# Performance work log

Measured on AMD Instinct MI355X. Metric: run time of the kernel, lower is better.

Reference implementation:

```python
import jax, jax.numpy as jnp
import numpy as np

FA, FB_CAT, FM, HID = 133, 147, 8, 100  # atom feat, bond feat (concat), mol feat, hidden
N_ATOMS, N_BONDS, N_MOLS, MAX_NB = 250000, 500000, 10000, 6
DEPTH = 3


def setup_inputs() -> dict:
    key = jax.random.key(0)
    ks = jax.random.split(key, 10)
    f_atoms = jax.random.normal(ks[0], (N_ATOMS, FA), jnp.float32)
    f_bonds = jax.random.normal(ks[1], (N_BONDS, FB_CAT), jnp.float32)
    f_mol = jax.random.normal(ks[2], (N_MOLS, FM), jnp.float32)
    a2b = jax.random.randint(ks[3], (N_ATOMS, MAX_NB), 0, N_BONDS, jnp.int32)
    b2a = jax.random.randint(ks[4], (N_BONDS,), 0, N_ATOMS, jnp.int32)
    b2revb = jax.random.randint(ks[5], (N_BONDS,), 0, N_BONDS, jnp.int32)
    # contiguous molecules of 25 atoms each -> equivalent of ascope segments
    mol_id = (jnp.arange(N_ATOMS, dtype=jnp.int32) // (N_ATOMS // N_MOLS))
    # parameters (Linear with bias=False): stored as (in, out)
    W_i = jax.random.normal(ks[6], (FB_CAT, HID), jnp.float32) * 0.05
    W_h = jax.random.normal(ks[7], (HID, HID), jnp.float32) * 0.05
    W_o = jax.random.normal(ks[8], (HID + FA, HID), jnp.float32) * 0.05
    return {"f_atoms": f_atoms, "f_bonds": f_bonds, "f_mol": f_mol,
            "W_i": W_i, "W_h": W_h, "W_o": W_o,
            "a2b": a2b, "b2a": b2a, "b2revb": b2revb,
            "mol_id": mol_id, "n_mols": N_MOLS}


def reference(f_atoms, f_bonds, f_mol, W_i, W_h, W_o, a2b, b2a, b2revb, mol_id, n_mols):
    act = jax.nn.relu
    inp = act(f_bonds @ W_i)              # (B, H)
    message = inp
    for _ in range(DEPTH - 1):
        nei = message[a2b]                # (A, MAX_NB, H) gather
        a_message = nei.sum(axis=1)       # (A, H)
        message = a_message[b2a] - message[b2revb]  # (B, H)
        message = act(inp + message @ W_h)
        # dropout p=0 (eval) -> identity
    # readout to atoms
    a_message = message[a2b].sum(axis=1)  # (A, H)
    a_input = jnp.concatenate([f_atoms, a_message], axis=1)  # (A, FA+H)
    atom_hiddens = act(a_input @ W_o)     # (A, H)
    # per-molecule mean over ragged segments (ascope equivalent)
    mol_sum = jax.ops.segment_sum(atom_hiddens, mol_id, num_segments=n_mols)
    counts = jax.ops.segment_sum(jnp.ones((atom_hiddens.shape[0],), atom_hiddens.dtype),
                                 mol_id, num_segments=n_mols)
    mol_vecs = mol_sum / jnp.maximum(counts, 1.0)[:, None]  # zero-vec for empty mols
    mol_vecs = jnp.concatenate([mol_vecs, f_mol], axis=1)   # (M, H+FM)
    return mol_vecs, atom_hiddens
```

## Files before the change

### kernel.cpp

```cpp
#include <hip/hip_runtime.h>

#define THREADS 256
#define MS 128

typedef __bf16 bf16x8 __attribute__((ext_vector_type(8)));
typedef float f32x4 __attribute__((ext_vector_type(4)));
typedef float f32x4u __attribute__((ext_vector_type(4), aligned(4)));

__device__ __forceinline__ unsigned short f2b(float x) {
    unsigned int u = __float_as_uint(x);
    u = (u + 0x7FFFu + ((u >> 16) & 1u)) >> 16;
    return (unsigned short)u;
}
__device__ __forceinline__ float b2f(unsigned short h) {
    return __uint_as_float(((unsigned int)h) << 16);
}
__device__ __forceinline__ bf16x8 as_bf(uint4 q) {
    union { uint4 q; bf16x8 v; } u; u.q = q; return u.v;
}

__global__ __launch_bounds__(64) void pack_w(const float* __restrict__ W,
                                             unsigned short* __restrict__ out, int K)
{
    int bid = blockIdx.x;
    int kc = bid / 7, nt = bid - kc * 7;
    int l = threadIdx.x;
    int k0 = kc * 32 + (l >> 4) * 8;
    int n = nt * 16 + (l & 15);
    unsigned short v[8];
    #pragma unroll
    for (int j = 0; j < 8; ++j) {
        int k = k0 + j;
        float x = (k < K && n < 100) ? W[(size_t)k * 100 + n] : 0.f;
        v[j] = f2b(x);
    }
    *(uint4*)&out[((size_t)bid * 64 + l) * 8] = *(uint4*)v;
}

__global__ __launch_bounds__(64) void pack_wo(const float* __restrict__ W,
                                              unsigned short* __restrict__ out)
{
    int bid = blockIdx.x;
    int kc = bid / 7, nt = bid - kc * 7;
    int l = threadIdx.x;
    int k0 = kc * 32 + (l >> 4) * 8;
    int n = nt * 16 + (l & 15);
    unsigned short v[8];
    #pragma unroll
    for (int j = 0; j < 8; ++j) {
        int k = k0 + j;
        float x = 0.f;
        if (n < 100) {
            if (k < 100)                 x = W[(size_t)(133 + k) * 100 + n];
            else if (k >= 112 && k < 245) x = W[(size_t)(k - 112) * 100 + n];
        }
        v[j] = f2b(x);
    }
    *(uint4*)&out[((size_t)bid * 64 + l) * 8] = *(uint4*)v;
}

__global__ __launch_bounds__(THREADS) void gather_sum_bf16(
    const unsigned short* __restrict__ msg, const int* __restrict__ a2b,
    unsigned short* __restrict__ amsg, int A)
{
    int t = blockIdx.x * THREADS + threadIdx.x;
    if (t >= A * 16) return;
    int a = t >> 4;
    int c = t & 15;
    if (c >= 14) {
        *(uint4*)&amsg[(size_t)a * MS + c * 8] = make_uint4(0u, 0u, 0u, 0u);
        return;
    }
    const int* nb = a2b + (size_t)a * 6;
    float s[8];
    #pragma unroll
    for (int e = 0; e < 8; ++e) s[e] = 0.f;
    #pragma unroll
    for (int j = 0; j < 6; ++j) {
        uint4 v = *(const uint4*)&msg[(size_t)nb[j] * MS + c * 8];
        const unsigned short* pv = (const unsigned short*)&v;
        #pragma unroll
        for (int e = 0; e < 8; ++e) s[e] += b2f(pv[e]);
    }
    unsigned short r[8];
    #pragma unroll
    for (int e = 0; e < 8; ++e) r[e] = f2b(s[e]);
    *(uint4*)&amsg[(size_t)a * MS + c * 8] = *(uint4*)r;
}

__global__ __launch_bounds__(THREADS) void gemm_in(
    const float* __restrict__ fb, const unsigned short* __restrict__ wf,
    unsigned short* __restrict__ Y, int M)
{
    __shared__ unsigned short Os[64 * 136];
    const int tid = threadIdx.x;
    const int l = tid & 63, w = tid >> 6;
    const int quad = l >> 4, c15 = l & 15;
    const int row0 = blockIdx.x * 64;
    const int rc = min(row0 + w * 16 + c15, M - 1);
    const float* rowp = fb + (size_t)rc * 147;

    uint4 af[5];
    #pragma unroll
    for (int kc = 0; kc < 4; ++kc) {
        f32x4u x0 = *(const f32x4u*)(rowp + kc * 32 + quad * 8);
        f32x4u x1 = *(const f32x4u*)(rowp + kc * 32 + quad * 8 + 4);
        unsigned short t[8];
        #pragma unroll
        for (int e = 0; e < 4; ++e) { t[e] = f2b(x0[e]); t[4 + e] = f2b(x1[e]); }
        af[kc] = *(uint4*)t;
    }
    {
        unsigned short t[8];
        #pragma unroll
        for (int j = 0; j < 8; ++j) {
            int k = 128 + quad * 8 + j;
            t[j] = (k < 147) ? f2b(rowp[k]) : (unsigned short)0;
        }
        af[4] = *(uint4*)t;
    }

    f32x4 acc[7];
    #pragma unroll
    for (int nt = 0; nt < 7; ++nt) acc[nt] = (f32x4){0.f, 0.f, 0.f, 0.f};
    #pragma unroll
    for (int kc = 0; kc < 5; ++kc) {
        #pragma unroll
        for (int nt = 0; nt < 7; ++nt) {
            uint4 bq = *(const uint4*)&wf[((size_t)(kc * 7 + nt) * 64 + l) * 8];
            acc[nt] = __builtin_amdgcn_mfma_f32_16x16x32_bf16(as_bf(af[kc]), as_bf(bq), acc[nt], 0, 0, 0);
        }
    }

    #pragma unroll
    for (int nt = 0; nt < 7; ++nt)
        #pragma unroll
        for (int reg = 0; reg < 4; ++reg)
            Os[(w * 16 + quad * 4 + reg) * 136 + nt * 16 + c15] = f2b(fmaxf(acc[nt][reg], 0.f));
    __syncthreads();

    for (int t = tid; t < 64 * 16; t += THREADS) {
        int rl = t >> 4, c = t & 15;
        int rr = row0 + rl;
        if (rr < M) {
            uint4 o = (c < 14) ? *(const uint4*)&Os[rl * 136 + c * 8]
                               : make_uint4(0u, 0u, 0u, 0u);
            *(uint4*)&Y[(size_t)rr * MS + c * 8] = o;
        }
    }
}

__global__ __launch_bounds__(THREADS) void gemm_msg(
    const unsigned short* __restrict__ amsg, const unsigned short* __restrict__ msg,
    const int* __restrict__ b2a, const int* __restrict__ b2revb,
    const unsigned short* __restrict__ wf, const unsigned short* __restrict__ bias,
    unsigned short* __restrict__ Y, int M)
{
    __shared__ unsigned short Os[64 * 136];
    const int tid = threadIdx.x;
    const int l = tid & 63, w = tid >> 6;
    const int quad = l >> 4, c15 = l & 15;
    const int row0 = blockIdx.x * 64;
    const int rc = min(row0 + w * 16 + c15, M - 1);
    const int iA = b2a[rc], iB = b2revb[rc];
    const unsigned short* pa = amsg + (size_t)iA * MS + quad * 8;
    const unsigned short* pb = msg  + (size_t)iB * MS + quad * 8;

    uint4 a1[4], a2[4];
    #pragma unroll
    for (int kc = 0; kc < 4; ++kc) {
        a1[kc] = *(const uint4*)(pa + kc * 32);
        a2[kc] = *(const uint4*)(pb + kc * 32);
    }

    f32x4 acc1[7], acc2[7];
    #pragma unroll
    for (int nt = 0; nt < 7; ++nt) {
        acc1[nt] = (f32x4){0.f, 0.f, 0.f, 0.f};
        acc2[nt] = (f32x4){0.f, 0.f, 0.f, 0.f};
    }
    #pragma unroll
    for (int kc = 0; kc < 4; ++kc) {
        #pragma unroll
        for (int nt = 0; nt < 7; ++nt) {
            uint4 bq = *(const uint4*)&wf[((size_t)(kc * 7 + nt) * 64 + l) * 8];
            acc1[nt] = __builtin_amdgcn_mfma_f32_16x16x32_bf16(as_bf(a1[kc]), as_bf(bq), acc1[nt], 0, 0, 0);
            acc2[nt] = __builtin_amdgcn_mfma_f32_16x16x32_bf16(as_bf(a2[kc]), as_bf(bq), acc2[nt], 0, 0, 0);
        }
    }

    #pragma unroll
    for (int nt = 0; nt < 7; ++nt)
        #pragma unroll
        for (int reg = 0; reg < 4; ++reg)
            Os[(w * 16 + quad * 4 + reg) * 136 + nt * 16 + c15] = f2b(acc1[nt][reg] - acc2[nt][reg]);
    __syncthreads();

    for (int t = tid; t < 64 * 16; t += THREADS) {
        int rl = t >> 4, c = t & 15;
        int rr = row0 + rl;
        if (rr >= M) continue;
        if (c < 14) {
            uint4 o = *(const uint4*)&Os[rl * 136 + c * 8];
            uint4 bq = *(const uint4*)&bias[(size_t)rr * MS + c * 8];
            const unsigned short* po = (const unsigned short*)&o;
            const unsigned short* pq = (const unsigned short*)&bq;
            unsigned short res[8];
            #pragma unroll
            for (int e = 0; e < 8; ++e)
                res[e] = f2b(fmaxf(b2f(po[e]) + b2f(pq[e]), 0.f));
            *(uint4*)&Y[(size_t)rr * MS + c * 8] = *(uint4*)res;
        } else {
            *(uint4*)&Y[(size_t)rr * MS + c * 8] = make_uint4(0u, 0u, 0u, 0u);
        }
    }
}

__global__ __launch_bounds__(THREADS) void gemm_out(
    const float* __restrict__ fa, const unsigned short* __restrict__ msg,
    const int* __restrict__ a2b,
    const unsigned short* __restrict__ wf, float* __restrict__ Y, int M)
{
    constexpr int KS = 264;
    __shared__ char smem[64 * KS * 2];
    unsigned short* Xs = (unsigned short*)smem;
    float* Os = (float*)smem;

    const int tid = threadIdx.x;
    const int l = tid & 63, w = tid >> 6;
    const int quad = l >> 4, c15 = l & 15;
    const int row0 = blockIdx.x * 64;

    for (int t = tid; t < 64 * 33; t += THREADS) {
        int rl = t / 33, c = t - rl * 33;
        int rr = min(row0 + rl, M - 1);
        uint4 o;
        if (c < 14) {
            const int* nb = a2b + (size_t)rr * 6;
            float s[8];
            #pragma unroll
            for (int e = 0; e < 8; ++e) s[e] = 0.f;
            #pragma unroll
            for (int j = 0; j < 6; ++j) {
                uint4 v = *(const uint4*)&msg[(size_t)nb[j] * MS + c * 8];
                const unsigned short* pv = (const unsigned short*)&v;
                #pragma unroll
                for (int e = 0; e < 8; ++e) s[e] += b2f(pv[e]);
            }
            unsigned short r[8];
            #pragma unroll
            for (int e = 0; e < 8; ++e) r[e] = f2b(s[e]);
            o = *(uint4*)r;
        } else if (c < 30) {
            int cc = c - 14;
            f32x4u x0 = *(const f32x4u*)(fa + (size_t)rr * 133 + cc * 8);
            f32x4u x1 = *(const f32x4u*)(fa + (size_t)rr * 133 + cc * 8 + 4);
            unsigned short tt[8];
            #pragma unroll
            for (int e = 0; e < 4; ++e) { tt[e] = f2b(x0[e]); tt[4 + e] = f2b(x1[e]); }
            o = *(uint4*)tt;
        } else if (c == 30) {
            unsigned short tt[8];
            #pragma unroll
            for (int j = 0; j < 8; ++j) {
                int col = 128 + j;
                tt[j] = (col < 133) ? f2b(fa[(size_t)rr * 133 + col]) : (unsigned short)0;
            }
            o = *(uint4*)tt;
        } else {
            o = make_uint4(0u, 0u, 0u, 0u);
        }
        *(uint4*)&Xs[(size_t)rl * KS + c * 8] = o;
    }
    __syncthreads();

    f32x4 acc[7];
    #pragma unroll
    for (int nt = 0; nt < 7; ++nt) acc[nt] = (f32x4){0.f, 0.f, 0.f, 0.f};
    const unsigned short* xrow = Xs + (size_t)(w * 16 + c15) * KS + quad * 8;
    #pragma unroll
    for (int kc = 0; kc < 8; ++kc) {
        bf16x8 av = *(const bf16x8*)(xrow + kc * 32);
        #pragma unroll
        for (int nt = 0; nt < 7; ++nt) {
            uint4 bq = *(const uint4*)&wf[((size_t)(kc * 7 + nt) * 64 + l) * 8];
            acc[nt] = __builtin_amdgcn_mfma_f32_16x16x32_bf16(av, as_bf(bq), acc[nt], 0, 0, 0);
        }
    }
    __syncthreads();

    #pragma unroll
    for (int nt = 0; nt < 7; ++nt) {
        int n = nt * 16 + c15;
        if (n < 100) {
            #pragma unroll
            for (int reg = 0; reg < 4; ++reg)
                Os[(w * 16 + quad * 4 + reg) * 108 + n] = fmaxf(acc[nt][reg], 0.f);
        }
    }
    __syncthreads();

    for (int t = tid; t < 64 * 25; t += THREADS) {
        int rl = t / 25, c = t - rl * 25;
        int rr = row0 + rl;
        if (rr < M)
            *(f32x4*)&Y[(size_t)rr * 100 + c * 4] = *(const f32x4*)&Os[rl * 108 + c * 4];
    }
}

__global__ __launch_bounds__(128) void readout(
    const float* __restrict__ atom_h, const float* __restrict__ f_mol,
    const int* __restrict__ mol_id, int n_atoms, float* __restrict__ out_mol)
{
    int m = blockIdx.x;
    int lo = 0, hi = n_atoms;
    while (lo < hi) { int mid = (lo + hi) >> 1; if (mol_id[mid] < m) lo = mid + 1; else hi = mid; }
    int lo2 = lo, hi2 = n_atoms;
    while (lo2 < hi2) { int mid = (lo2 + hi2) >> 1; if (mol_id[mid] < m + 1) lo2 = mid + 1; else hi2 = mid; }
    float inv = 1.0f / fmaxf((float)(lo2 - lo), 1.0f);
    int c = threadIdx.x;
    if (c < 100) {
        float s = 0.f;
        for (int a = lo; a < lo2; ++a) s += atom_h[(size_t)a * 100 + c];
        out_mol[(size_t)m * 108 + c] = s * inv;
    } else if (c < 108) {
        out_mol[(size_t)m * 108 + c] = f_mol[(size_t)m * 8 + (c - 100)];
    }
}

extern "C" void kernel_launch(void* const* d_in, const int* in_sizes, int n_in,
                              void* d_out, int out_size, void* d_ws, size_t ws_size,
                              hipStream_t stream)
{
    const float* f_atoms = (const float*)d_in[0];
    const float* f_bonds = (const float*)d_in[1];
    const float* f_mol   = (const float*)d_in[2];
    const float* W_i     = (const float*)d_in[3];
    const float* W_h     = (const float*)d_in[4];
    const float* W_o     = (const float*)d_in[5];
    const int* a2b    = (const int*)d_in[6];
    const int* b2a    = (const int*)d_in[7];
    const int* b2revb = (const int*)d_in[8];
    const int* mol_id = (const int*)d_in[9];

    const int A    = in_sizes[0] / 133;
    const int B    = in_sizes[1] / 147;
    const int Mmol = in_sizes[2] / 8;

    unsigned short* wsu = (unsigned short*)d_ws;
    unsigned short* wfi  = wsu;
    unsigned short* wfh  = wfi + 35 * 512;
    unsigned short* wfo  = wfh + 28 * 512;
    unsigned short* amsg = wfo + 56 * 512;
    unsigned short* inp  = amsg + (size_t)A * MS;
    unsigned short* msgA = inp  + (size_t)B * MS;
    unsigned short* msgB = msgA + (size_t)B * MS;

    float* out     = (float*)d_out;
    float* out_mol = out;
    float* atom_h  = out + (size_t)Mmol * 108;

    dim3 blk(THREADS);
    int gB = (B + 63) / 64;
    int gA = (A + 63) / 64;
    int gg = (A * 16 + THREADS - 1) / THREADS;

    pack_w<<<35, dim3(64), 0, stream>>>(W_i, wfi, 147);
    pack_w<<<28, dim3(64), 0, stream>>>(W_h, wfh, 100);
    pack_wo<<<56, dim3(64), 0, stream>>>(W_o, wfo);

    gemm_in<<<gB, blk, 0, stream>>>(f_bonds, wfi, inp, B);

    gather_sum_bf16<<<gg, blk, 0, stream>>>(inp, a2b, amsg, A);
    gemm_msg<<<gB, blk, 0, stream>>>(amsg, inp, b2a, b2revb, wfh, inp, msgA, B);

    gather_sum_bf16<<<gg, blk, 0, stream>>>(msgA, a2b, amsg, A);
    gemm_msg<<<gB, blk, 0, stream>>>(amsg, msgA, b2a, b2revb, wfh, inp, msgB, B);

    gemm_out<<<gA, blk, 0, stream>>>(f_atoms, msgB, a2b, wfo, atom_h, A);

    readout<<<Mmol, dim3(128), 0, stream>>>(atom_h, f_mol, mol_id, A, out_mol);
}
```

Measured before the change: 1.041 ms.

## Fuse readout segment-sum into gemm_out via atomics, merge pack kernels, add nontemporal loads

Combines the three weight-packing kernels and a zeroing of the molecule output into a single prep kernel. The per-molecule sum moves into gemm_out's epilogue: each block sums its rows per molecule and atomically adds them into out_mol, leaving a light finalize kernel that only scales by the atom count and copies f_mol. Streaming inputs and outputs now use nontemporal loads and stores, and the last gemm_msg skips writing the padding columns. This removes the re-read of atom_hiddens and the serial per-molecule loop, at the cost of float atomics that make the summation order nondeterministic.

```diff
diff --git a/kernel.cpp b/kernel.cpp
--- a/kernel.cpp
+++ b/kernel.cpp
@@ -6,6 +6,7 @@
 typedef __bf16 bf16x8 __attribute__((ext_vector_type(8)));
 typedef float f32x4 __attribute__((ext_vector_type(4)));
 typedef float f32x4u __attribute__((ext_vector_type(4), aligned(4)));
+typedef unsigned int u32x4 __attribute__((ext_vector_type(4)));
 
 __device__ __forceinline__ unsigned short f2b(float x) {
     unsigned int u = __float_as_uint(x);
@@ -18,13 +19,19 @@
 __device__ __forceinline__ bf16x8 as_bf(uint4 q) {
     union { uint4 q; bf16x8 v; } u; u.q = q; return u.v;
 }
-
-__global__ __launch_bounds__(64) void pack_w(const float* __restrict__ W,
-                                             unsigned short* __restrict__ out, int K)
-{
-    int bid = blockIdx.x;
+__device__ __forceinline__ f32x4u nt4(const float* p) {
+    return __builtin_nontemporal_load((const f32x4u*)p);
+}
+__device__ __forceinline__ uint4 ntq(const unsigned short* p) {
+    u32x4 v = __builtin_nontemporal_load((const u32x4*)p);
+    return make_uint4(v.x, v.y, v.z, v.w);
+}
+
+__device__ __forceinline__ void pack_body(const float* __restrict__ W,
+                                          unsigned short* __restrict__ out,
+                                          int K, int bid, int l)
+{
     int kc = bid / 7, nt = bid - kc * 7;
-    int l = threadIdx.x;
     int k0 = kc * 32 + (l >> 4) * 8;
     int n = nt * 16 + (l & 15);
     unsigned short v[8];
@@ -37,12 +44,11 @@
     *(uint4*)&out[((size_t)bid * 64 + l) * 8] = *(uint4*)v;
 }
 
-__global__ __launch_bounds__(64) void pack_wo(const float* __restrict__ W,
-                                              unsigned short* __restrict__ out)
-{
-    int bid = blockIdx.x;
+__device__ __forceinline__ void pack_wo_body(const float* __restrict__ W,
+                                             unsigned short* __restrict__ out,
+                                             int bid, int l)
+{
     int kc = bid / 7, nt = bid - kc * 7;
-    int l = threadIdx.x;
     int k0 = kc * 32 + (l >> 4) * 8;
     int n = nt * 16 + (l & 15);
     unsigned short v[8];
@@ -51,12 +57,33 @@
         int k = k0 + j;
         float x = 0.f;
         if (n < 100) {
-            if (k < 100)                 x = W[(size_t)(133 + k) * 100 + n];
+            if (k < 100)                  x = W[(size_t)(133 + k) * 100 + n];
             else if (k >= 112 && k < 245) x = W[(size_t)(k - 112) * 100 + n];
         }
         v[j] = f2b(x);
     }
     *(uint4*)&out[((size_t)bid * 64 + l) * 8] = *(uint4*)v;
+}
+
+__global__ __launch_bounds__(64) void prep(
+    const float* __restrict__ Wi, const float* __restrict__ Wh, const float* __restrict__ Wo,
+    unsigned short* __restrict__ wfi, unsigned short* __restrict__ wfh,
+    unsigned short* __restrict__ wfo, float* __restrict__ out_mol, int nmol_floats)
+{
+    int bid = blockIdx.x;
+    int l = threadIdx.x;
+    if (bid < 35) {
+        pack_body(Wi, wfi, 147, bid, l);
+    } else if (bid < 63) {
+        pack_body(Wh, wfh, 100, bid - 35, l);
+    } else if (bid < 119) {
+        pack_wo_body(Wo, wfo, bid - 63, l);
+    } else {
+        int idx = (bid - 119) * 64 + l;
+        int stride = (gridDim.x - 119) * 64;
+        for (int i = idx; i * 4 < nmol_floats; i += stride)
+            *(f32x4*)&out_mol[(size_t)i * 4] = (f32x4){0.f, 0.f, 0.f, 0.f};
+    }
 }
 
 __global__ __launch_bounds__(THREADS) void gather_sum_bf16(
@@ -103,8 +130,8 @@
     uint4 af[5];
     #pragma unroll
     for (int kc = 0; kc < 4; ++kc) {
-        f32x4u x0 = *(const f32x4u*)(rowp + kc * 32 + quad * 8);
-        f32x4u x1 = *(const f32x4u*)(rowp + kc * 32 + quad * 8 + 4);
+        f32x4u x0 = nt4(rowp + kc * 32 + quad * 8);
+        f32x4u x1 = nt4(rowp + kc * 32 + quad * 8 + 4);
         unsigned short t[8];
         #pragma unroll
         for (int e = 0; e < 4; ++e) { t[e] = f2b(x0[e]); t[4 + e] = f2b(x1[e]); }
@@ -115,7 +142,7 @@
         #pragma unroll
         for (int j = 0; j < 8; ++j) {
             int k = 128 + quad * 8 + j;
-            t[j] = (k < 147) ? f2b(rowp[k]) : (unsigned short)0;
+            t[j] = (k < 147) ? f2b(__builtin_nontemporal_load(rowp + k)) : (unsigned short)0;
         }
         af[4] = *(uint4*)t;
     }
@@ -154,7 +181,7 @@
     const unsigned short* __restrict__ amsg, const unsigned short* __restrict__ msg,
     const int* __restrict__ b2a, const int* __restrict__ b2revb,
     const unsigned short* __restrict__ wf, const unsigned short* __restrict__ bias,
-    unsigned short* __restrict__ Y, int M)
+    unsigned short* __restrict__ Y, int M, int last)
 {
     __shared__ unsigned short Os[64 * 136];
     const int tid = threadIdx.x;
@@ -202,7 +229,8 @@
         if (rr >= M) continue;
         if (c < 14) {
             uint4 o = *(const uint4*)&Os[rl * 136 + c * 8];
-            uint4 bq = *(const uint4*)&bias[(size_t)rr * MS + c * 8];
+            uint4 bq = last ? ntq(&bias[(size_t)rr * MS + c * 8])
+                            : *(const uint4*)&bias[(size_t)rr * MS + c * 8];
             const unsigned short* po = (const unsigned short*)&o;
             const unsigned short* pq = (const unsigned short*)&bq;
             unsigned short res[8];
@@ -210,7 +238,7 @@
             for (int e = 0; e < 8; ++e)
                 res[e] = f2b(fmaxf(b2f(po[e]) + b2f(pq[e]), 0.f));
             *(uint4*)&Y[(size_t)rr * MS + c * 8] = *(uint4*)res;
-        } else {
+        } else if (!last) {
             *(uint4*)&Y[(size_t)rr * MS + c * 8] = make_uint4(0u, 0u, 0u, 0u);
         }
     }
@@ -218,11 +246,13 @@
 
 __global__ __launch_bounds__(THREADS) void gemm_out(
     const float* __restrict__ fa, const unsigned short* __restrict__ msg,
-    const int* __restrict__ a2b,
-    const unsigned short* __restrict__ wf, float* __restrict__ Y, int M)
+    const int* __restrict__ a2b, const unsigned short* __restrict__ wf,
+    const int* __restrict__ mol_id, float* __restrict__ Y,
+    float* __restrict__ out_mol, int M)
 {
     constexpr int KS = 264;
     __shared__ char smem[64 * KS * 2];
+    __shared__ int mids[64];
     unsigned short* Xs = (unsigned short*)smem;
     float* Os = (float*)smem;
 
@@ -230,6 +260,11 @@
     const int l = tid & 63, w = tid >> 6;
     const int quad = l >> 4, c15 = l & 15;
     const int row0 = blockIdx.x * 64;
+
+    if (tid < 64) {
+        int rr = row0 + tid;
+        mids[tid] = (rr < M) ? mol_id[rr] : -1;
+    }
 
     for (int t = tid; t < 64 * 33; t += THREADS) {
         int rl = t / 33, c = t - rl * 33;
@@ -253,8 +288,8 @@
             o = *(uint4*)r;
         } else if (c < 30) {
             int cc = c - 14;
-            f32x4u x0 = *(const f32x4u*)(fa + (size_t)rr * 133 + cc * 8);
-            f32x4u x1 = *(const f32x4u*)(fa + (size_t)rr * 133 + cc * 8 + 4);
+            f32x4u x0 = nt4(fa + (size_t)rr * 133 + cc * 8);
+            f32x4u x1 = nt4(fa + (size_t)rr * 133 + cc * 8 + 4);
             unsigned short tt[8];
             #pragma unroll
             for (int e = 0; e < 4; ++e) { tt[e] = f2b(x0[e]); tt[4 + e] = f2b(x1[e]); }
@@ -264,7 +299,8 @@
             #pragma unroll
             for (int j = 0; j < 8; ++j) {
                 int col = 128 + j;
-                tt[j] = (col < 133) ? f2b(fa[(size_t)rr * 133 + col]) : (unsigned short)0;
+                tt[j] = (col < 133) ? f2b(__builtin_nontemporal_load(fa + (size_t)rr * 133 + col))
+                                    : (unsigned short)0;
             }
             o = *(uint4*)tt;
         } else {
@@ -304,13 +340,32 @@
         int rl = t / 25, c = t - rl * 25;
         int rr = row0 + rl;
         if (rr < M)
-            *(f32x4*)&Y[(size_t)rr * 100 + c * 4] = *(const f32x4*)&Os[rl * 108 + c * 4];
-    }
-}
-
-__global__ __launch_bounds__(128) void readout(
-    const float* __restrict__ atom_h, const float* __restrict__ f_mol,
-    const int* __restrict__ mol_id, int n_atoms, float* __restrict__ out_mol)
+            __builtin_nontemporal_store(*(const f32x4*)&Os[rl * 108 + c * 4],
+                                        (f32x4*)&Y[(size_t)rr * 100 + c * 4]);
+    }
+
+    if (tid < 100) {
+        int c = tid;
+        float s = 0.f;
+        int cur = mids[0];
+        #pragma unroll 1
+        for (int rl = 0; rl < 64; ++rl) {
+            int mid = mids[rl];
+            if (mid != cur) {
+                if (cur >= 0) atomicAdd(&out_mol[(size_t)cur * 108 + c], s);
+                s = 0.f;
+                cur = mid;
+            }
+            if (mid < 0) break;
+            s += Os[rl * 108 + c];
+        }
+        if (cur >= 0) atomicAdd(&out_mol[(size_t)cur * 108 + c], s);
+    }
+}
+
+__global__ __launch_bounds__(128) void finalize(
+    float* __restrict__ out_mol, const float* __restrict__ f_mol,
+    const int* __restrict__ mol_id, int n_atoms)
 {
     int m = blockIdx.x;
     int lo = 0, hi = n_atoms;
@@ -320,9 +375,7 @@
     float inv = 1.0f / fmaxf((float)(lo2 - lo), 1.0f);
     int c = threadIdx.x;
     if (c < 100) {
-        float s = 0.f;
-        for (int a = lo; a < lo2; ++a) s += atom_h[(size_t)a * 100 + c];
-        out_mol[(size_t)m * 108 + c] = s * inv;
+        out_mol[(size_t)m * 108 + c] *= inv;
     } else if (c < 108) {
         out_mol[(size_t)m * 108 + c] = f_mol[(size_t)m * 8 + (c - 100)];
     }
@@ -365,19 +418,18 @@
     int gA = (A + 63) / 64;
     int gg = (A * 16 + THREADS - 1) / THREADS;
 
-    pack_w<<<35, dim3(64), 0, stream>>>(W_i, wfi, 147);
-    pack_w<<<28, dim3(64), 0, stream>>>(W_h, wfh, 100);
-    pack_wo<<<56, dim3(64), 0, stream>>>(W_o, wfo);
+    prep<<<119 + 256, dim3(64), 0, stream>>>(W_i, W_h, W_o, wfi, wfh, wfo,
+                                             out_mol, Mmol * 108);
 
     gemm_in<<<gB, blk, 0, stream>>>(f_bonds, wfi, inp, B);
 
     gather_sum_bf16<<<gg, blk, 0, stream>>>(inp, a2b, amsg, A);
-    gemm_msg<<<gB, blk, 0, stream>>>(amsg, inp, b2a, b2revb, wfh, inp, msgA, B);
+    gemm_msg<<<gB, blk, 0, stream>>>(amsg, inp, b2a, b2revb, wfh, inp, msgA, B, 0);
 
     gather_sum_bf16<<<gg, blk, 0, stream>>>(msgA, a2b, amsg, A);
-    gemm_msg<<<gB, blk, 0, stream>>>(amsg, msgA, b2a, b2revb, wfh, inp, msgB, B);
-
-    gemm_out<<<gA, blk, 0, stream>>>(f_atoms, msgB, a2b, wfo, atom_h, A);
-
-    readout<<<Mmol, dim3(128), 0, stream>>>(atom_h, f_mol, mol_id, A, out_mol);
-}
+    gemm_msg<<<gB, blk, 0, stream>>>(amsg, msgA, b2a, b2revb, wfh, inp, msgB, B, 1);
+
+    gemm_out<<<gA, blk, 0, stream>>>(f_atoms, msgB, a2b, wfo, mol_id, atom_h, out_mol, A);
+
+    finalize<<<Mmol, dim3(128), 0, stream>>>(out_mol, f_mol, mol_id, A);
+}
```

Result: slower. 1.099 ms (+5.6%).
